# Performance work log

Hardware: AMD Instinct MI355X
Metric: run time of the kernel (lower is better)

The kernel has to match this reference:

```python
import jax, jax.numpy as jnp
import numpy as np

N_POI = 100_000
N_EDGE = 50_000
NNZ = 3_200_000
D = 128
NUM_LAYERS = 2


def setup_inputs() -> dict:
    key = jax.random.key(0)
    ks = jax.random.split(key, 11)
    return {
        "poi_embs": jax.random.normal(ks[0], (N_POI, D), jnp.float32),
        "edge_embs": jax.random.normal(ks[1], (N_EDGE, D), jnp.float32),
        "W_poi": jax.random.normal(ks[2], (D, D), jnp.float32) * 0.05,
        "W_edge": jax.random.normal(ks[3], (D, D), jnp.float32) * 0.05,
        "W_fus": jax.random.normal(ks[4], (D, 2 * D), jnp.float32) * 0.05,
        "p2e_row": jax.random.randint(ks[5], (NNZ,), 0, N_EDGE, jnp.int32),
        "p2e_col": jax.random.randint(ks[6], (NNZ,), 0, N_POI, jnp.int32),
        "p2e_val": jax.random.uniform(ks[7], (NNZ,), jnp.float32),
        "e2p_row": jax.random.randint(ks[8], (NNZ,), 0, N_POI, jnp.int32),
        "e2p_col": jax.random.randint(ks[9], (NNZ,), 0, N_EDGE, jnp.int32),
        "e2p_val": jax.random.uniform(ks[10], (NNZ,), jnp.float32),
    }


def _spmm(rows, cols, vals, x, num_segments):
    # COO sparse [num_segments, x.shape[0]] @ x : gather rows, scale, scatter-add.
    return jax.ops.segment_sum(vals[:, None] * x[cols], rows, num_segments=num_segments)


def reference(poi_embs, edge_embs, W_poi, W_edge, W_fus,
              p2e_row, p2e_col, p2e_val, e2p_row, e2p_col, e2p_val):
    # dropout p = 0.0 -> identity
    poi_acc = [poi_embs]
    edge_acc = [edge_embs]
    p, e = poi_embs, edge_embs
    for _ in range(NUM_LAYERS):
        poi_msg = _spmm(p2e_row, p2e_col, p2e_val, p @ W_poi.T, N_EDGE)   # [N_edge, D]
        edge_msg = e @ W_edge.T                                           # [N_edge, D]
        fused = jnp.concatenate([poi_msg, edge_msg], axis=1) @ W_fus.T    # [N_edge, D]
        prop = _spmm(e2p_row, e2p_col, e2p_val, fused, N_POI)             # [N_poi, D]
        p = prop + poi_acc[-1]
        e = fused + edge_acc[-1]
        poi_acc.append(p)
        edge_acc.append(e)
    poi_out = jnp.mean(jnp.stack(poi_acc), axis=0)
    edge_out = jnp.mean(jnp.stack(edge_acc), axis=0)
    return (poi_out, edge_out)
```

## Files before the change

### kernel.cpp

```cpp
#include <hip/hip_runtime.h>

#define N_POI 100000
#define N_EDGE 50000
#define NNZ 3200000
#define D 128

#define NBKT 196
#define SH_P2E 8
#define SH_E2P 9
#define PTILE 4000
#define PGRID 800

__device__ inline unsigned short f2bf(float f) {
    unsigned int u = __float_as_uint(f);
    return (unsigned short)((u + 0x7fff + ((u >> 16) & 1)) >> 16);
}
__device__ inline float bf2f(unsigned short u) {
    return __uint_as_float(((unsigned int)u) << 16);
}
__device__ inline int2 nt_int2(const int2* p) {
    unsigned long long u = __builtin_nontemporal_load((const unsigned long long*)p);
    int2 r; r.x = (int)(unsigned)(u & 0xffffffffull); r.y = (int)(unsigned)(u >> 32);
    return r;
}

__global__ __launch_bounds__(128) void wcombo_kernel(const float* __restrict__ Wpoi,
                                                     const float* __restrict__ Wedge,
                                                     const float* __restrict__ Wfus,
                                                     float* __restrict__ WdT,
                                                     float* __restrict__ WcT) {
    int i = blockIdx.x;
    int j = threadIdx.x;
    float s1 = 0.f, s2 = 0.f;
    for (int k = 0; k < D; ++k) {
        float f1 = Wfus[i * 256 + k];
        float f2 = Wfus[i * 256 + 128 + k];
        s1 += f1 * Wpoi[k * D + j];
        s2 += f2 * Wedge[k * D + j];
    }
    WdT[j * D + i] = s1;
    WcT[j * D + i] = s2;
}

template <bool BF16OUT>
__global__ __launch_bounds__(256) void dense_xmT(const float* __restrict__ X,
                                                 const float* __restrict__ MT,
                                                 void* __restrict__ Yv, int nrows) {
    __shared__ float mt[D * D];
    __shared__ float xs[32 * D];
    for (int i = threadIdx.x; i < D * D / 4; i += 256)
        ((float4*)mt)[i] = ((const float4*)MT)[i];

    int ntiles = (nrows + 31) >> 5;
    int rg = threadIdx.x >> 5;
    int cg = threadIdx.x & 31;
    int r0 = rg * 4;
    int c0 = cg * 4;

    for (int tile = blockIdx.x; tile < ntiles; tile += gridDim.x) {
        int rbase = tile * 32;
        int nr = min(32, nrows - rbase);
        __syncthreads();
        for (int i = threadIdx.x; i < nr * 32; i += 256)
            ((float4*)xs)[i] = ((const float4*)(X + (size_t)rbase * D))[i];
        __syncthreads();

        float4 a0 = {0, 0, 0, 0}, a1 = {0, 0, 0, 0}, a2 = {0, 0, 0, 0}, a3 = {0, 0, 0, 0};
#pragma unroll 4
        for (int k = 0; k < D; ++k) {
            float4 m = *(const float4*)&mt[k * D + c0];
            float x0 = xs[(r0 + 0) * D + k];
            float x1 = xs[(r0 + 1) * D + k];
            float x2 = xs[(r0 + 2) * D + k];
            float x3 = xs[(r0 + 3) * D + k];
            a0.x += x0 * m.x; a0.y += x0 * m.y; a0.z += x0 * m.z; a0.w += x0 * m.w;
            a1.x += x1 * m.x; a1.y += x1 * m.y; a1.z += x1 * m.z; a1.w += x1 * m.w;
            a2.x += x2 * m.x; a2.y += x2 * m.y; a2.z += x2 * m.z; a2.w += x2 * m.w;
            a3.x += x3 * m.x; a3.y += x3 * m.y; a3.z += x3 * m.z; a3.w += x3 * m.w;
        }
        float4 accs[4] = {a0, a1, a2, a3};
#pragma unroll
        for (int t = 0; t < 4; ++t) {
            if (r0 + t < nr) {
                size_t off = (size_t)(rbase + r0 + t) * D + c0;
                if (BF16OUT) {
                    ushort4 u;
                    u.x = f2bf(accs[t].x); u.y = f2bf(accs[t].y);
                    u.z = f2bf(accs[t].z); u.w = f2bf(accs[t].w);
                    *(ushort4*)&((unsigned short*)Yv)[off] = u;
                } else {
                    *(float4*)&((float*)Yv)[off] = accs[t];
                }
            }
        }
    }
}


__global__ __launch_bounds__(256) void bkt_count(const int* __restrict__ r, int sh,
                                                 int* __restrict__ tot) {
    __shared__ int h[NBKT];
    for (int i = threadIdx.x; i < NBKT; i += 256) h[i] = 0;
    __syncthreads();
    const int4* r4 = (const int4*)r;
    const int n4 = NNZ / 4;
    for (int k = blockIdx.x * 256 + threadIdx.x; k < n4; k += gridDim.x * 256) {
        int4 rr = r4[k];
        atomicAdd(&h[rr.x >> sh], 1);
        atomicAdd(&h[rr.y >> sh], 1);
        atomicAdd(&h[rr.z >> sh], 1);
        atomicAdd(&h[rr.w >> sh], 1);
    }
    __syncthreads();
    for (int i = threadIdx.x; i < NBKT; i += 256)
        if (h[i]) atomicAdd(&tot[i], h[i]);
}

__global__ __launch_bounds__(256) void bkt_scan(const int* __restrict__ tot,
                                                int* __restrict__ base,
                                                int* __restrict__ gcur,
                                                int* __restrict__ rp, int nrows) {
    __shared__ int buf[256];
    int v = (threadIdx.x < NBKT) ? tot[threadIdx.x] : 0;
    buf[threadIdx.x] = v;
    __syncthreads();
    for (int off = 1; off < 256; off <<= 1) {
        int t = (threadIdx.x >= off) ? buf[threadIdx.x - off] : 0;
        __syncthreads();
        buf[threadIdx.x] += t;
        __syncthreads();
    }
    int excl = buf[threadIdx.x] - v;
    if (threadIdx.x < NBKT) { base[threadIdx.x] = excl; gcur[threadIdx.x] = excl; }
    if (threadIdx.x == 0) { base[NBKT] = NNZ; rp[nrows] = NNZ; }
}

__global__ __launch_bounds__(256) void partition_kernel(
    const int* __restrict__ r, const int* __restrict__ c, const float* __restrict__ v,
    int* __restrict__ gcur, int sh, int* __restrict__ rb, int2* __restrict__ cvb) {
    __shared__ int hist[NBKT];
    __shared__ int excl[NBKT];
    __shared__ int cur[NBKT];
    __shared__ int runb[NBKT];
    __shared__ int sbuf[256];
    __shared__ int rs[PTILE];
    __shared__ int2 cvs[PTILE];
    const int base = blockIdx.x * PTILE;
    for (int i = threadIdx.x; i < NBKT; i += 256) hist[i] = 0;
    __syncthreads();
    const int4* r4 = (const int4*)(r + base);
    for (int k = threadIdx.x; k < PTILE / 4; k += 256) {
        int4 rr = r4[k];
        atomicAdd(&hist[rr.x >> sh], 1);
        atomicAdd(&hist[rr.y >> sh], 1);
        atomicAdd(&hist[rr.z >> sh], 1);
        atomicAdd(&hist[rr.w >> sh], 1);
    }
    __syncthreads();
    int hv = (threadIdx.x < NBKT) ? hist[threadIdx.x] : 0;
    sbuf[threadIdx.x] = hv;
    __syncthreads();
    for (int off = 1; off < 256; off <<= 1) {
        int t = (threadIdx.x >= off) ? sbuf[threadIdx.x - off] : 0;
        __syncthreads();
        sbuf[threadIdx.x] += t;
        __syncthreads();
    }
    if (threadIdx.x < NBKT) {
        int e = sbuf[threadIdx.x] - hv;
        excl[threadIdx.x] = e;
        cur[threadIdx.x] = e;
        runb[threadIdx.x] = hv ? atomicAdd(&gcur[threadIdx.x], hv) : 0;
    }
    __syncthreads();
    const int4* c4 = (const int4*)(c + base);
    const float4* v4 = (const float4*)(v + base);
    for (int k = threadIdx.x; k < PTILE / 4; k += 256) {
        int4 rr = r4[k];
        int4 cc = c4[k];
        float4 vv = v4[k];
        int p;
        p = atomicAdd(&cur[rr.x >> sh], 1); rs[p] = rr.x; cvs[p] = make_int2(cc.x, __float_as_int(vv.x));
        p = atomicAdd(&cur[rr.y >> sh], 1); rs[p] = rr.y; cvs[p] = make_int2(cc.y, __float_as_int(vv.y));
        p = atomicAdd(&cur[rr.z >> sh], 1); rs[p] = rr.z; cvs[p] = make_int2(cc.z, __float_as_int(vv.z));
        p = atomicAdd(&cur[rr.w >> sh], 1); rs[p] = rr.w; cvs[p] = make_int2(cc.w, __float_as_int(vv.w));
    }
    __syncthreads();
    for (int p = threadIdx.x; p < PTILE; p += 256) {
        int row = rs[p];
        int b = row >> sh;
        int dst = runb[b] + (p - excl[b]);
        rb[dst] = row;
        cvb[dst] = cvs[p];
    }
}

__global__ __launch_bounds__(512) void bucket_scatter(
    const int* __restrict__ base, const int* __restrict__ rb, const int2* __restrict__ cvb,
    int sh, int nrows, int* __restrict__ rp, int2* __restrict__ cv) {
    __shared__ int cur[512];
    __shared__ int sbuf[512];
    const int b = blockIdx.x;
    const int s0 = base[b];
    const int n = base[b + 1] - s0;
    const int row0 = b << sh;
    const int nr = min(1 << sh, nrows - row0);
    for (int i = threadIdx.x; i < (1 << sh); i += 512) cur[i] = 0;
    __syncthreads();
    for (int k = threadIdx.x; k < n; k += 512)
        atomicAdd(&cur[rb[s0 + k] - row0], 1);
    __syncthreads();
    int cnt = (threadIdx.x < (1 << sh)) ? cur[threadIdx.x] : 0;
    sbuf[threadIdx.x] = cnt;
    __syncthreads();
    for (int off = 1; off < 512; off <<= 1) {
        int t = (threadIdx.x >= off) ? sbuf[threadIdx.x - off] : 0;
        __syncthreads();
        sbuf[threadIdx.x] += t;
        __syncthreads();
    }
    if (threadIdx.x < (1 << sh)) {
        int e = s0 + sbuf[threadIdx.x] - cnt;
        cur[threadIdx.x] = e;
        if (threadIdx.x < nr) rp[row0 + threadIdx.x] = e;
    }
    __syncthreads();
    for (int k = threadIdx.x; k < n; k += 512) {
        int row = rb[s0 + k];
        int p = atomicAdd(&cur[row - row0], 1);
        cv[p] = cvb[s0 + k];
    }
}

template <bool HAS_Y, bool HAS_B1, bool HAS_OB>
__global__ __launch_bounds__(256) void spmm_csr_fused(
    const int* __restrict__ row_ptr, const int2* __restrict__ cv,
    const unsigned short* __restrict__ Xb, const float* __restrict__ Yinit,
    const float* __restrict__ base0, const float* __restrict__ base1,
    float* __restrict__ outF, unsigned short* __restrict__ outb,
    float c0, float c1, float c2, int nrows) {
    int row = (blockIdx.x * 256 + threadIdx.x) >> 5;
    int lane = threadIdx.x & 31;
    if (row >= nrows) return;
    int j = row_ptr[row];
    int end = row_ptr[row + 1];
    size_t off = (size_t)row * D + lane * 4;

    float4 acc = {0, 0, 0, 0};
    if (HAS_Y) acc = *(const float4*)&Yinit[off];

    for (; j + 8 <= end; j += 8) {
        int2 e[8];
#pragma unroll
        for (int t = 0; t < 8; ++t) e[t] = nt_int2(&cv[j + t]);
        ushort4 x[8];
#pragma unroll
        for (int t = 0; t < 8; ++t)
            x[t] = *(const ushort4*)&Xb[(size_t)e[t].x * D + lane * 4];
#pragma unroll
        for (int t = 0; t < 8; ++t) {
            float v = __int_as_float(e[t].y);
            acc.x += v * bf2f(x[t].x); acc.y += v * bf2f(x[t].y);
            acc.z += v * bf2f(x[t].z); acc.w += v * bf2f(x[t].w);
        }
    }
    for (; j < end; ++j) {
        int2 a = nt_int2(&cv[j]);
        float va = __int_as_float(a.y);
        ushort4 xa = *(const ushort4*)&Xb[(size_t)a.x * D + lane * 4];
        acc.x += va * bf2f(xa.x); acc.y += va * bf2f(xa.y);
        acc.z += va * bf2f(xa.z); acc.w += va * bf2f(xa.w);
    }

    float4 b0 = *(const float4*)&base0[off];
    float4 o;
    o.x = c0 * b0.x + c2 * acc.x;
    o.y = c0 * b0.y + c2 * acc.y;
    o.z = c0 * b0.z + c2 * acc.z;
    o.w = c0 * b0.w + c2 * acc.w;
    if (HAS_B1) {
        float4 b1 = *(const float4*)&base1[off];
        o.x += c1 * b1.x; o.y += c1 * b1.y; o.z += c1 * b1.z; o.w += c1 * b1.w;
    }
    *(float4*)&outF[off] = o;
    if (HAS_OB) {
        ushort4 u;
        u.x = f2bf(acc.x); u.y = f2bf(acc.y); u.z = f2bf(acc.z); u.w = f2bf(acc.w);
        *(ushort4*)&outb[off] = u;
    }
}

extern "C" void kernel_launch(void* const* d_in, const int* in_sizes, int n_in,
                              void* d_out, int out_size, void* d_ws, size_t ws_size,
                              hipStream_t stream) {
    const float* poi   = (const float*)d_in[0];
    const float* edge  = (const float*)d_in[1];
    const float* Wpoi  = (const float*)d_in[2];
    const float* Wedge = (const float*)d_in[3];
    const float* Wfus  = (const float*)d_in[4];
    const int*   p2e_row = (const int*)d_in[5];
    const int*   p2e_col = (const int*)d_in[6];
    const float* p2e_val = (const float*)d_in[7];
    const int*   e2p_row = (const int*)d_in[8];
    const int*   e2p_col = (const int*)d_in[9];
    const float* e2p_val = (const float*)d_in[10];

    float* out_poi  = (float*)d_out;
    float* out_edge = out_poi + (size_t)N_POI * D;

    char* w = (char*)d_ws;
    unsigned short* Ab = (unsigned short*)w; w += (size_t)N_POI * D * 2;
    float* B           = (float*)w;          w += (size_t)N_EDGE * D * 4;
    unsigned short* Bb = (unsigned short*)w; w += (size_t)N_EDGE * D * 2;
    float* p_cur       = (float*)w;          w += (size_t)N_POI * D * 4;
    float* e_cur       = (float*)w;          w += (size_t)N_EDGE * D * 4;
    float* WdT         = (float*)w;          w += D * D * 4;
    float* WcT         = (float*)w;          w += D * D * 4;
    int*   rp_p2e      = (int*)w;            w += ((N_EDGE + 1) * 4 + 15) / 16 * 16;
    int*   rp_e2p      = (int*)w;            w += ((N_POI + 1) * 4 + 15) / 16 * 16;
    int*   bkt_tot     = (int*)w;            w += 256 * 4;
    int*   bkt_base    = (int*)w;            w += 256 * 4;
    int*   bkt_cur     = (int*)w;            w += 256 * 4;
    int2*  cv_p2e      = (int2*)w;           w += (size_t)NNZ * 8;
    int2*  cv_e2p      = (int2*)w;           w += (size_t)NNZ * 8;

    int*  rb_g  = (int*)Ab;
    int2* cvb_g = (int2*)B;

    wcombo_kernel<<<128, 128, 0, stream>>>(Wpoi, Wedge, Wfus, WdT, WcT);

    hipMemsetAsync(bkt_tot, 0, NBKT * sizeof(int), stream);
    bkt_count<<<256, 256, 0, stream>>>(p2e_row, SH_P2E, bkt_tot);
    bkt_scan<<<1, 256, 0, stream>>>(bkt_tot, bkt_base, bkt_cur, rp_p2e, N_EDGE);
    partition_kernel<<<PGRID, 256, 0, stream>>>(p2e_row, p2e_col, p2e_val, bkt_cur,
                                                SH_P2E, rb_g, cvb_g);
    bucket_scatter<<<NBKT, 512, 0, stream>>>(bkt_base, rb_g, cvb_g, SH_P2E, N_EDGE,
                                             rp_p2e, cv_p2e);

    hipMemsetAsync(bkt_tot, 0, NBKT * sizeof(int), stream);
    bkt_count<<<256, 256, 0, stream>>>(e2p_row, SH_E2P, bkt_tot);
    bkt_scan<<<1, 256, 0, stream>>>(bkt_tot, bkt_base, bkt_cur, rp_e2p, N_POI);
    partition_kernel<<<PGRID, 256, 0, stream>>>(e2p_row, e2p_col, e2p_val, bkt_cur,
                                                SH_E2P, rb_g, cvb_g);
    bucket_scatter<<<NBKT, 512, 0, stream>>>(bkt_base, rb_g, cvb_g, SH_E2P, N_POI,
                                             rp_e2p, cv_e2p);

    const float T = 1.f / 3.f;

    dense_xmT<true><<<512, 256, 0, stream>>>(poi, WdT, Ab, N_POI);
    dense_xmT<false><<<512, 256, 0, stream>>>(edge, WcT, B, N_EDGE);
    spmm_csr_fused<true, false, true><<<(N_EDGE + 7) / 8, 256, 0, stream>>>(
        rp_p2e, cv_p2e, Ab, B, edge, nullptr, e_cur, Bb, 1.f, 0.f, 1.f, N_EDGE);
    spmm_csr_fused<false, false, false><<<(N_POI + 7) / 8, 256, 0, stream>>>(
        rp_e2p, cv_e2p, Bb, nullptr, poi, nullptr, p_cur, nullptr, 1.f, 0.f, 1.f, N_POI);

    dense_xmT<true><<<512, 256, 0, stream>>>(p_cur, WdT, Ab, N_POI);
    dense_xmT<false><<<512, 256, 0, stream>>>(e_cur, WcT, B, N_EDGE);
    spmm_csr_fused<true, true, true><<<(N_EDGE + 7) / 8, 256, 0, stream>>>(
        rp_p2e, cv_p2e, Ab, B, edge, e_cur, out_edge, Bb, T, 2.f * T, T, N_EDGE);
    spmm_csr_fused<false, true, false><<<(N_POI + 7) / 8, 256, 0, stream>>>(
        rp_e2p, cv_e2p, Bb, nullptr, poi, p_cur, out_poi, nullptr, T, 2.f * T, T, N_POI);
}
```

Baseline: 1.060 ms.

## Batch both COO-to-CSR conversions into shared launches and use nontemporal loads/stores

Merges the p2e and e2p bucket count, scan, partition and scatter kernels so each launch handles both matrices, using separate scratch buffers (e_cur/p_cur reused as staging). This halves the number of preprocessing launches and lets the two conversions fill the GPU together instead of running back to back. Bucket scatter now uses 1024-thread blocks. Separately, SpMM kernels use nontemporal loads for Yinit and nontemporal stores for final outputs to reduce cache pollution. Risk: larger blocks may lower occupancy, and the reused scratch buffers must not overlap live data.

```diff
diff --git a/kernel.cpp b/kernel.cpp
--- a/kernel.cpp
+++ b/kernel.cpp
@@ -22,6 +22,15 @@
     unsigned long long u = __builtin_nontemporal_load((const unsigned long long*)p);
     int2 r; r.x = (int)(unsigned)(u & 0xffffffffull); r.y = (int)(unsigned)(u >> 32);
     return r;
+}
+typedef float fvec4 __attribute__((ext_vector_type(4)));
+__device__ inline float4 nt_ld_f4(const float* p) {
+    fvec4 v = __builtin_nontemporal_load((const fvec4*)p);
+    return make_float4(v[0], v[1], v[2], v[3]);
+}
+__device__ inline void nt_st_f4(float* p, float4 v) {
+    fvec4 t; t[0] = v.x; t[1] = v.y; t[2] = v.z; t[3] = v.w;
+    __builtin_nontemporal_store(t, (fvec4*)p);
 }
 
 __global__ __launch_bounds__(128) void wcombo_kernel(const float* __restrict__ Wpoi,
@@ -97,14 +106,22 @@
 }
 
 
-__global__ __launch_bounds__(256) void bkt_count(const int* __restrict__ r, int sh,
-                                                 int* __restrict__ tot) {
+__global__ __launch_bounds__(256) void bkt_count2(const int* __restrict__ r0,
+                                                  const int* __restrict__ r1,
+                                                  int* __restrict__ tot0,
+                                                  int* __restrict__ tot1) {
     __shared__ int h[NBKT];
+    const int half = gridDim.x >> 1;
+    const bool second = blockIdx.x >= half;
+    const int* r = second ? r1 : r0;
+    int* tot = second ? tot1 : tot0;
+    const int sh = second ? SH_E2P : SH_P2E;
+    const int bid = second ? blockIdx.x - half : blockIdx.x;
     for (int i = threadIdx.x; i < NBKT; i += 256) h[i] = 0;
     __syncthreads();
     const int4* r4 = (const int4*)r;
     const int n4 = NNZ / 4;
-    for (int k = blockIdx.x * 256 + threadIdx.x; k < n4; k += gridDim.x * 256) {
+    for (int k = bid * 256 + threadIdx.x; k < n4; k += half * 256) {
         int4 rr = r4[k];
         atomicAdd(&h[rr.x >> sh], 1);
         atomicAdd(&h[rr.y >> sh], 1);
@@ -116,11 +133,19 @@
         if (h[i]) atomicAdd(&tot[i], h[i]);
 }
 
-__global__ __launch_bounds__(256) void bkt_scan(const int* __restrict__ tot,
-                                                int* __restrict__ base,
-                                                int* __restrict__ gcur,
-                                                int* __restrict__ rp, int nrows) {
+__global__ __launch_bounds__(256) void bkt_scan2(const int* __restrict__ tot0,
+                                                 int* __restrict__ baseA, int* __restrict__ curA,
+                                                 int* __restrict__ rpA,
+                                                 const int* __restrict__ tot1,
+                                                 int* __restrict__ baseB, int* __restrict__ curB,
+                                                 int* __restrict__ rpB) {
     __shared__ int buf[256];
+    const bool second = blockIdx.x == 1;
+    const int* tot = second ? tot1 : tot0;
+    int* base = second ? baseB : baseA;
+    int* gcur = second ? curB : curA;
+    int* rp = second ? rpB : rpA;
+    const int nrows = second ? N_POI : N_EDGE;
     int v = (threadIdx.x < NBKT) ? tot[threadIdx.x] : 0;
     buf[threadIdx.x] = v;
     __syncthreads();
@@ -135,9 +160,11 @@
     if (threadIdx.x == 0) { base[NBKT] = NNZ; rp[nrows] = NNZ; }
 }
 
-__global__ __launch_bounds__(256) void partition_kernel(
-    const int* __restrict__ r, const int* __restrict__ c, const float* __restrict__ v,
-    int* __restrict__ gcur, int sh, int* __restrict__ rb, int2* __restrict__ cvb) {
+__global__ __launch_bounds__(256) void partition2(
+    const int* __restrict__ r0, const int* __restrict__ c0, const float* __restrict__ v0,
+    int* __restrict__ gcur0, int* __restrict__ rbA, int2* __restrict__ cvbA,
+    const int* __restrict__ r1, const int* __restrict__ c1, const float* __restrict__ v1,
+    int* __restrict__ gcur1, int* __restrict__ rbB, int2* __restrict__ cvbB) {
     __shared__ int hist[NBKT];
     __shared__ int excl[NBKT];
     __shared__ int cur[NBKT];
@@ -145,7 +172,17 @@
     __shared__ int sbuf[256];
     __shared__ int rs[PTILE];
     __shared__ int2 cvs[PTILE];
-    const int base = blockIdx.x * PTILE;
+    const bool second = blockIdx.x >= PGRID;
+    const int bid = second ? blockIdx.x - PGRID : blockIdx.x;
+    const int* r = second ? r1 : r0;
+    const int* c = second ? c1 : c0;
+    const float* v = second ? v1 : v0;
+    int* gcur = second ? gcur1 : gcur0;
+    int* rb = second ? rbB : rbA;
+    int2* cvb = second ? cvbB : cvbA;
+    const int sh = second ? SH_E2P : SH_P2E;
+
+    const int base = bid * PTILE;
     for (int i = threadIdx.x; i < NBKT; i += 256) hist[i] = 0;
     __syncthreads();
     const int4* r4 = (const int4*)(r + base);
@@ -195,25 +232,36 @@
     }
 }
 
-__global__ __launch_bounds__(512) void bucket_scatter(
-    const int* __restrict__ base, const int* __restrict__ rb, const int2* __restrict__ cvb,
-    int sh, int nrows, int* __restrict__ rp, int2* __restrict__ cv) {
+__global__ __launch_bounds__(1024) void bucket_scatter2(
+    const int* __restrict__ baseA, const int* __restrict__ rbA, const int2* __restrict__ cvbA,
+    int* __restrict__ rpA, int2* __restrict__ cvA,
+    const int* __restrict__ baseB, const int* __restrict__ rbB, const int2* __restrict__ cvbB,
+    int* __restrict__ rpB, int2* __restrict__ cvB) {
     __shared__ int cur[512];
-    __shared__ int sbuf[512];
-    const int b = blockIdx.x;
+    __shared__ int sbuf[1024];
+    const bool second = blockIdx.x >= NBKT;
+    const int b = second ? blockIdx.x - NBKT : blockIdx.x;
+    const int* base = second ? baseB : baseA;
+    const int* rb = second ? rbB : rbA;
+    const int2* cvb = second ? cvbB : cvbA;
+    int* rp = second ? rpB : rpA;
+    int2* cv = second ? cvB : cvA;
+    const int sh = second ? SH_E2P : SH_P2E;
+    const int nrows = second ? N_POI : N_EDGE;
+
     const int s0 = base[b];
     const int n = base[b + 1] - s0;
     const int row0 = b << sh;
     const int nr = min(1 << sh, nrows - row0);
-    for (int i = threadIdx.x; i < (1 << sh); i += 512) cur[i] = 0;
-    __syncthreads();
-    for (int k = threadIdx.x; k < n; k += 512)
+    for (int i = threadIdx.x; i < (1 << sh); i += 1024) cur[i] = 0;
+    __syncthreads();
+    for (int k = threadIdx.x; k < n; k += 1024)
         atomicAdd(&cur[rb[s0 + k] - row0], 1);
     __syncthreads();
     int cnt = (threadIdx.x < (1 << sh)) ? cur[threadIdx.x] : 0;
     sbuf[threadIdx.x] = cnt;
     __syncthreads();
-    for (int off = 1; off < 512; off <<= 1) {
+    for (int off = 1; off < 1024; off <<= 1) {
         int t = (threadIdx.x >= off) ? sbuf[threadIdx.x - off] : 0;
         __syncthreads();
         sbuf[threadIdx.x] += t;
@@ -225,14 +273,14 @@
         if (threadIdx.x < nr) rp[row0 + threadIdx.x] = e;
     }
     __syncthreads();
-    for (int k = threadIdx.x; k < n; k += 512) {
+    for (int k = threadIdx.x; k < n; k += 1024) {
         int row = rb[s0 + k];
         int p = atomicAdd(&cur[row - row0], 1);
         cv[p] = cvb[s0 + k];
     }
 }
 
-template <bool HAS_Y, bool HAS_B1, bool HAS_OB>
+template <bool HAS_Y, bool HAS_B1, bool HAS_OB, bool NTOUT>
 __global__ __launch_bounds__(256) void spmm_csr_fused(
     const int* __restrict__ row_ptr, const int2* __restrict__ cv,
     const unsigned short* __restrict__ Xb, const float* __restrict__ Yinit,
@@ -247,7 +295,7 @@
     size_t off = (size_t)row * D + lane * 4;
 
     float4 acc = {0, 0, 0, 0};
-    if (HAS_Y) acc = *(const float4*)&Yinit[off];
+    if (HAS_Y) acc = nt_ld_f4(&Yinit[off]);
 
     for (; j + 8 <= end; j += 8) {
         int2 e[8];
@@ -282,7 +330,8 @@
         float4 b1 = *(const float4*)&base1[off];
         o.x += c1 * b1.x; o.y += c1 * b1.y; o.z += c1 * b1.z; o.w += c1 * b1.w;
     }
-    *(float4*)&outF[off] = o;
+    if (NTOUT) nt_st_f4(&outF[off], o);
+    else       *(float4*)&outF[off] = o;
     if (HAS_OB) {
         ushort4 u;
         u.x = f2bf(acc.x); u.y = f2bf(acc.y); u.z = f2bf(acc.z); u.w = f2bf(acc.w);
@@ -318,46 +367,44 @@
     float* WcT         = (float*)w;          w += D * D * 4;
     int*   rp_p2e      = (int*)w;            w += ((N_EDGE + 1) * 4 + 15) / 16 * 16;
     int*   rp_e2p      = (int*)w;            w += ((N_POI + 1) * 4 + 15) / 16 * 16;
-    int*   bkt_tot     = (int*)w;            w += 256 * 4;
-    int*   bkt_base    = (int*)w;            w += 256 * 4;
-    int*   bkt_cur     = (int*)w;            w += 256 * 4;
+    int*   bkt_tot     = (int*)w;            w += 512 * 4;
+    int*   bkt_base    = (int*)w;            w += 512 * 4;
+    int*   bkt_cur     = (int*)w;            w += 512 * 4;
     int2*  cv_p2e      = (int2*)w;           w += (size_t)NNZ * 8;
     int2*  cv_e2p      = (int2*)w;           w += (size_t)NNZ * 8;
 
-    int*  rb_g  = (int*)Ab;
-    int2* cvb_g = (int2*)B;
+    int* tot0 = bkt_tot;        int* tot1 = bkt_tot + 256;
+    int* baseA = bkt_base;      int* baseB = bkt_base + 256;
+    int* curA = bkt_cur;        int* curB = bkt_cur + 256;
+
+    int*  rbA  = (int*)Ab;
+    int2* cvbA = (int2*)B;
+    int*  rbB  = (int*)e_cur;
+    int2* cvbB = (int2*)p_cur;
 
     wcombo_kernel<<<128, 128, 0, stream>>>(Wpoi, Wedge, Wfus, WdT, WcT);
 
-    hipMemsetAsync(bkt_tot, 0, NBKT * sizeof(int), stream);
-    bkt_count<<<256, 256, 0, stream>>>(p2e_row, SH_P2E, bkt_tot);
-    bkt_scan<<<1, 256, 0, stream>>>(bkt_tot, bkt_base, bkt_cur, rp_p2e, N_EDGE);
-    partition_kernel<<<PGRID, 256, 0, stream>>>(p2e_row, p2e_col, p2e_val, bkt_cur,
-                                                SH_P2E, rb_g, cvb_g);
-    bucket_scatter<<<NBKT, 512, 0, stream>>>(bkt_base, rb_g, cvb_g, SH_P2E, N_EDGE,
-                                             rp_p2e, cv_p2e);
-
-    hipMemsetAsync(bkt_tot, 0, NBKT * sizeof(int), stream);
-    bkt_count<<<256, 256, 0, stream>>>(e2p_row, SH_E2P, bkt_tot);
-    bkt_scan<<<1, 256, 0, stream>>>(bkt_tot, bkt_base, bkt_cur, rp_e2p, N_POI);
-    partition_kernel<<<PGRID, 256, 0, stream>>>(e2p_row, e2p_col, e2p_val, bkt_cur,
-                                                SH_E2P, rb_g, cvb_g);
-    bucket_scatter<<<NBKT, 512, 0, stream>>>(bkt_base, rb_g, cvb_g, SH_E2P, N_POI,
-                                             rp_e2p, cv_e2p);
+    hipMemsetAsync(bkt_tot, 0, 512 * sizeof(int), stream);
+    bkt_count2<<<512, 256, 0, stream>>>(p2e_row, e2p_row, tot0, tot1);
+    bkt_scan2<<<2, 256, 0, stream>>>(tot0, baseA, curA, rp_p2e, tot1, baseB, curB, rp_e2p);
+    partition2<<<2 * PGRID, 256, 0, stream>>>(p2e_row, p2e_col, p2e_val, curA, rbA, cvbA,
+                                              e2p_row, e2p_col, e2p_val, curB, rbB, cvbB);
+    bucket_scatter2<<<2 * NBKT, 1024, 0, stream>>>(baseA, rbA, cvbA, rp_p2e, cv_p2e,
+                                                   baseB, rbB, cvbB, rp_e2p, cv_e2p);
 
     const float T = 1.f / 3.f;
 
     dense_xmT<true><<<512, 256, 0, stream>>>(poi, WdT, Ab, N_POI);
     dense_xmT<false><<<512, 256, 0, stream>>>(edge, WcT, B, N_EDGE);
-    spmm_csr_fused<true, false, true><<<(N_EDGE + 7) / 8, 256, 0, stream>>>(
+    spmm_csr_fused<true, false, true, false><<<(N_EDGE + 7) / 8, 256, 0, stream>>>(
         rp_p2e, cv_p2e, Ab, B, edge, nullptr, e_cur, Bb, 1.f, 0.f, 1.f, N_EDGE);
-    spmm_csr_fused<false, false, false><<<(N_POI + 7) / 8, 256, 0, stream>>>(
+    spmm_csr_fused<false, false, false, false><<<(N_POI + 7) / 8, 256, 0, stream>>>(
         rp_e2p, cv_e2p, Bb, nullptr, poi, nullptr, p_cur, nullptr, 1.f, 0.f, 1.f, N_POI);
 
     dense_xmT<true><<<512, 256, 0, stream>>>(p_cur, WdT, Ab, N_POI);
     dense_xmT<false><<<512, 256, 0, stream>>>(e_cur, WcT, B, N_EDGE);
-    spmm_csr_fused<true, true, true><<<(N_EDGE + 7) / 8, 256, 0, stream>>>(
+    spmm_csr_fused<true, true, true, true><<<(N_EDGE + 7) / 8, 256, 0, stream>>>(
         rp_p2e, cv_p2e, Ab, B, edge, e_cur, out_edge, Bb, T, 2.f * T, T, N_EDGE);
-    spmm_csr_fused<false, true, false><<<(N_POI + 7) / 8, 256, 0, stream>>>(
+    spmm_csr_fused<false, true, false, true><<<(N_POI + 7) / 8, 256, 0, stream>>>(
         rp_e2p, cv_e2p, Bb, nullptr, poi, p_cur, out_poi, nullptr, T, 2.f * T, T, N_POI);
 }
```

Result: faster. 994.3 us (-6.2%).
